# Optimization experiments

Measured on AMD Instinct MI355X. Metric: run time of the kernel, lower is better.

The kernel has to match this reference:

```python
import jax, jax.numpy as jnp
import numpy as np

B, T, N = 256, 512, 128  # batch, max seq len, num tags


def setup_inputs() -> dict:
    key = jax.random.key(0)
    k1, k2, k3, k4, k5, k6 = jax.random.split(key, 6)
    log_potentials = jax.random.normal(k1, (B, T, N), dtype=jnp.float32)
    transition = jax.random.normal(k2, (N, N), dtype=jnp.float32) * 0.01
    start_transition = jax.random.normal(k3, (N,), dtype=jnp.float32) * 0.01
    end_transition = jax.random.normal(k4, (N,), dtype=jnp.float32) * 0.01
    lengths = jax.random.randint(k5, (B,), T // 2, T + 1).astype(jnp.int32)
    target = jax.random.randint(k6, (B, T), 0, N).astype(jnp.int32)
    return {
        "log_potentials": log_potentials,
        "transition": transition,
        "start_transition": start_transition,
        "end_transition": end_transition,
        "target": target,
        "lengths": lengths,
    }


def _log_partitions(log_potentials, transition, start_transition, end_transition, lengths):
    # log-semiring forward algorithm over ragged (length-masked) sequences.
    emit = jnp.transpose(log_potentials, (1, 0, 2))  # [T, B, N]
    alpha0 = start_transition[None, :] + emit[0]     # log.mul(start, e_0)

    valid = (jnp.arange(1, emit.shape[0])[:, None] < lengths[None, :])  # [T-1, B]

    def step(alpha, inp):
        e_t, v_t = inp
        # log.vm: new[b, j] = logsumexp_i alpha[b, i] + transition[i, j] + e_t[b, j]
        new = jax.nn.logsumexp(alpha[:, :, None] + transition[None, :, :], axis=1) + e_t
        alpha = jnp.where(v_t[:, None], new, alpha)  # padded steps act as semiring unit
        return alpha, None

    alpha, _ = jax.lax.scan(step, alpha0, (emit[1:], valid))
    # log.mv with end transition
    return jax.nn.logsumexp(alpha + end_transition[None, :], axis=-1)  # [B]


def _log_scores(log_potentials, transition, start_transition, end_transition, target, lengths):
    Tn = log_potentials.shape[1]
    tidx = jnp.arange(Tn)
    valid = tidx[None, :] < lengths[:, None]  # [B, T]
    emis = jnp.take_along_axis(log_potentials, target[..., None].astype(jnp.int32), axis=-1)[..., 0]
    emis_score = jnp.sum(jnp.where(valid, emis, 0.0), axis=1)
    tr = transition[target[:, :-1], target[:, 1:]]
    tr_score = jnp.sum(jnp.where(valid[:, 1:], tr, 0.0), axis=1)
    last = jnp.take_along_axis(target, (lengths - 1)[:, None], axis=1)[:, 0]
    return emis_score + tr_score + start_transition[target[:, 0]] + end_transition[last]


def reference(log_potentials, transition, start_transition, end_transition, target, lengths):
    # CrfDecoderABC.fit -> CrfDistribution.log_prob = log_scores - log_partitions
    log_z = _log_partitions(log_potentials, transition, start_transition, end_transition, lengths)
    score = _log_scores(log_potentials, transition, start_transition, end_transition, target, lengths)
    return score - log_z  # [B]
```

## Files before the change

kernel.cpp:

```cpp
#include <hip/hip_runtime.h>

#define B_ 256
#define T_ 512
#define N_ 128

typedef float v2f __attribute__((ext_vector_type(2)));

__device__ __forceinline__ float readlane_f(float v, int k) {
    return __int_as_float(__builtin_amdgcn_readlane(__float_as_int(v), k));
}

__device__ __forceinline__ void barrier_lds() {
    asm volatile("s_waitcnt lgkmcnt(0)\n\ts_barrier" ::: "memory");
}

__global__ __launch_bounds__(256, 1) void crf_fused_kernel(
    const float* __restrict__ lp,
    const float* __restrict__ trans,
    const float* __restrict__ startt,
    const float* __restrict__ endt,
    const int*   __restrict__ target,
    const int*   __restrict__ lengths,
    float*       __restrict__ out)
{
    const int b   = blockIdx.x;
    const int tid = threadIdx.x;
    const int w   = tid >> 6;
    const int l   = tid & 63;
    const int lq  = l & 31;

    __shared__ v2f  part[2][4][64];
    __shared__ float red[8];

    const float* lpb = lp + (size_t)b * (T_ * N_);
    const int len = lengths[b];

    v2f e2[32];
    {
        const float* tq = trans + (w << 5) * N_;
        #pragma unroll
        for (int k = 0; k < 32; ++k) {
            e2[k] = (v2f){ __expf(tq[k * N_ + l]),
                           __expf(tq[k * N_ + 64 + l]) };
        }
    }

    float s = __expf(startt[(w << 5) + lq] + lpb[(w << 5) + lq]);

    float Macc = 0.f;

    const float* emb = lpb + (w << 5) + lq;
    float cur = emb[1 * N_], nA = emb[2 * N_], nB = emb[3 * N_];

    const int fi = ((((w & 1) << 5) + lq) << 1) + (w >> 1);

    for (int t = 1; t < len; ++t) {
        const int tp = min(t + 3, T_ - 1);
        float nn = emb[tp * N_];

        float eexp = __expf(cur);

        v2f a0 = {0.f, 0.f}, a1 = {0.f, 0.f}, a2 = {0.f, 0.f}, a3 = {0.f, 0.f};
        #pragma unroll
        for (int k = 0; k < 32; k += 4) {
            float x0 = readlane_f(s, k);
            float x1 = readlane_f(s, k + 1);
            float x2 = readlane_f(s, k + 2);
            float x3 = readlane_f(s, k + 3);
            a0 = __builtin_elementwise_fma(e2[k],     (v2f){x0, x0}, a0);
            a1 = __builtin_elementwise_fma(e2[k + 1], (v2f){x1, x1}, a1);
            a2 = __builtin_elementwise_fma(e2[k + 2], (v2f){x2, x2}, a2);
            a3 = __builtin_elementwise_fma(e2[k + 3], (v2f){x3, x3}, a3);
        }
        v2f p = (a0 + a1) + (a2 + a3);

        const int pb = t & 1;
        part[pb][w][l] = p;
        barrier_lds();

        const float* pbase = (const float*)&part[pb][0][0];
        float r0 = pbase[fi];
        float r1 = pbase[128 + fi];
        float r2 = pbase[256 + fi];
        float r3 = pbase[384 + fi];
        float sc4 = (r0 + r1) + (r2 + r3);

        if ((t & 3) == 0) {
            float scp = pbase[0];
            float isc = __builtin_amdgcn_rcpf(scp);
            sc4 *= isc;
            Macc += __logf(scp);
        }

        s = sc4 * eexp;

        cur = nA; nA = nB; nB = nn;
    }

    {
        float f = (l < 32) ? s * __expf(endt[(w << 5) + l]) : 0.f;
        #pragma unroll
        for (int off = 32; off > 0; off >>= 1) f += __shfl_xor(f, off);
        if (l == 0) red[w] = f;
    }

    const int* tg = target + b * T_;
    float acc = 0.f;
    for (int t = tid; t < len; t += 256) {
        int c = tg[t];
        acc += lpb[t * N_ + c];
        if (t + 1 < len) acc += trans[c * N_ + tg[t + 1]];
    }
    #pragma unroll
    for (int off = 32; off > 0; off >>= 1) acc += __shfl_xor(acc, off);
    if (l == 0) red[4 + w] = acc;
    __syncthreads();

    if (tid == 0) {
        float fz = (red[0] + red[1]) + (red[2] + red[3]);
        float sc = (red[4] + red[5]) + (red[6] + red[7]);
        out[b] = sc + startt[tg[0]] + endt[tg[len - 1]] - (Macc + __logf(fz));
    }
}

extern "C" void kernel_launch(void* const* d_in, const int* in_sizes, int n_in,
                              void* d_out, int out_size, void* d_ws, size_t ws_size,
                              hipStream_t stream) {
    const float* lp     = (const float*)d_in[0];
    const float* trans  = (const float*)d_in[1];
    const float* st     = (const float*)d_in[2];
    const float* en     = (const float*)d_in[3];
    const int*   target = (const int*)d_in[4];
    const int*   lens   = (const int*)d_in[5];
    float* out = (float*)d_out;

    crf_fused_kernel<<<B_, 256, 0, stream>>>(lp, trans, st, en, target, lens, out);
}
```

Baseline: 275.5 us.

## Run CRF forward recurrence on bf16 MFMA with expm1 transition split

Replaces the readlane-broadcast FP32 FMA matvec per time step with bf16 MFMA 16x16x32 instructions. The transition matrix is stored as expm1(trans) in bf16 and the identity part is added back exactly through the alpha sum (S*e), which keeps bf16 rounding error small. The state is exchanged through a small double-buffered LDS vector instead of partial-sum reduction, the loop is unrolled by two, and rescaling now uses an exponent-bit power-of-two shift in place of log/rcp. This cuts the VALU and readlane cost on the serial critical path, at the price of bf16 precision in the correction term and MFMA latency on each step.

```diff
diff --git a/kernel.cpp b/kernel.cpp
--- a/kernel.cpp
+++ b/kernel.cpp
@@ -4,12 +4,19 @@
 #define T_ 512
 #define N_ 128
 
-typedef float v2f __attribute__((ext_vector_type(2)));
+typedef float  f32x4 __attribute__((ext_vector_type(4)));
+typedef short  s16x8 __attribute__((ext_vector_type(8)));
+typedef unsigned int u32x4 __attribute__((ext_vector_type(4)));
 
-__device__ __forceinline__ float readlane_f(float v, int k) {
-    return __int_as_float(__builtin_amdgcn_readlane(__float_as_int(v), k));
+__device__ __forceinline__ unsigned int bf16_rne(float f) {
+    unsigned int u = __float_as_uint(f);
+    u += 0x7FFFu + ((u >> 16) & 1u);
+    return u >> 16;
 }
-
+__device__ __forceinline__ unsigned int pack_bf16(float lo, float hi) {
+    return __builtin_amdgcn_perm(__float_as_uint(hi), __float_as_uint(lo),
+                                 0x07060302u);
+}
 __device__ __forceinline__ void barrier_lds() {
     asm volatile("s_waitcnt lgkmcnt(0)\n\ts_barrier" ::: "memory");
 }
@@ -27,78 +34,101 @@
     const int tid = threadIdx.x;
     const int w   = tid >> 6;
     const int l   = tid & 63;
-    const int lq  = l & 31;
+    const int c   = l & 15;
+    const int g   = l >> 4;
+    const int gp  = g & 1;
 
-    __shared__ v2f  part[2][4][64];
+    __shared__ float xld[2][N_];
     __shared__ float red[8];
 
     const float* lpb = lp + (size_t)b * (T_ * N_);
     const int len = lengths[b];
 
-    v2f e2[32];
-    {
-        const float* tq = trans + (w << 5) * N_;
+    s16x8 Bf[4][2];
+    #pragma unroll
+    for (int kt = 0; kt < 4; ++kt) {
         #pragma unroll
-        for (int k = 0; k < 32; ++k) {
-            e2[k] = (v2f){ __expf(tq[k * N_ + l]),
-                           __expf(tq[k * N_ + 64 + l]) };
+        for (int jtl = 0; jtl < 2; ++jtl) {
+            const float* tq = trans + (32 * kt + 8 * g) * N_ + 16 * (2 * w + jtl) + c;
+            unsigned d0 = bf16_rne(expm1f(tq[0 * N_])) | (bf16_rne(expm1f(tq[1 * N_])) << 16);
+            unsigned d1 = bf16_rne(expm1f(tq[2 * N_])) | (bf16_rne(expm1f(tq[3 * N_])) << 16);
+            unsigned d2 = bf16_rne(expm1f(tq[4 * N_])) | (bf16_rne(expm1f(tq[5 * N_])) << 16);
+            unsigned d3 = bf16_rne(expm1f(tq[6 * N_])) | (bf16_rne(expm1f(tq[7 * N_])) << 16);
+            u32x4 u = { d0, d1, d2, d3 };
+            Bf[kt][jtl] = __builtin_bit_cast(s16x8, u);
         }
     }
 
-    float s = __expf(startt[(w << 5) + lq] + lpb[(w << 5) + lq]);
+    const int jsel = 32 * w + 16 * gp + c;
 
-    float Macc = 0.f;
+    float a_sel = __expf(startt[jsel] + lpb[jsel]);
+    if (l < 32) xld[0][32 * w + l] = a_sel;
 
-    const float* emb = lpb + (w << 5) + lq;
-    float cur = emb[1 * N_], nA = emb[2 * N_], nB = emb[3 * N_];
+    int Mexp = 0;
 
-    const int fi = ((((w & 1) << 5) + lq) << 1) + (w >> 1);
+    float emA = lpb[1 * N_ + jsel];
+    float emB = lpb[2 * N_ + jsel];
 
-    for (int t = 1; t < len; ++t) {
-        const int tp = min(t + 3, T_ - 1);
-        float nn = emb[tp * N_];
+    barrier_lds();
 
-        float eexp = __expf(cur);
+    auto step = [&](int t, float& em) {
+        const int pr = (t - 1) & 1;
+        const int pw = t & 1;
 
-        v2f a0 = {0.f, 0.f}, a1 = {0.f, 0.f}, a2 = {0.f, 0.f}, a3 = {0.f, 0.f};
+        s16x8 Af[4];
+        f32x4 sv = { 0.f, 0.f, 0.f, 0.f };
         #pragma unroll
-        for (int k = 0; k < 32; k += 4) {
-            float x0 = readlane_f(s, k);
-            float x1 = readlane_f(s, k + 1);
-            float x2 = readlane_f(s, k + 2);
-            float x3 = readlane_f(s, k + 3);
-            a0 = __builtin_elementwise_fma(e2[k],     (v2f){x0, x0}, a0);
-            a1 = __builtin_elementwise_fma(e2[k + 1], (v2f){x1, x1}, a1);
-            a2 = __builtin_elementwise_fma(e2[k + 2], (v2f){x2, x2}, a2);
-            a3 = __builtin_elementwise_fma(e2[k + 3], (v2f){x3, x3}, a3);
+        for (int kt = 0; kt < 4; ++kt) {
+            const f32x4* ls = (const f32x4*)&xld[pr][32 * kt + 8 * g];
+            f32x4 lo = ls[0], hi = ls[1];
+            sv += lo + hi;
+            u32x4 u = { pack_bf16(lo[0], lo[1]), pack_bf16(lo[2], lo[3]),
+                        pack_bf16(hi[0], hi[1]), pack_bf16(hi[2], hi[3]) };
+            Af[kt] = __builtin_bit_cast(s16x8, u);
         }
-        v2f p = (a0 + a1) + (a2 + a3);
+        float S = (sv[0] + sv[1]) + (sv[2] + sv[3]);
+        S += __shfl_xor(S, 16);
+        S += __shfl_xor(S, 32);
 
-        const int pb = t & 1;
-        part[pb][w][l] = p;
+        float ee = __expf(em);
+        em = lpb[(size_t)min(t + 2, T_ - 1) * N_ + jsel];
+
+        float e2 = ee;
+        if ((t & 3) == 0) {
+            unsigned eb = (__float_as_uint(S) >> 23) & 0xFFu;
+            e2 *= __uint_as_float((254u - eb) << 23);
+            Mexp += (int)eb - 127;
+        }
+        const float Se2 = S * e2;
+
+        f32x4 z = { 0.f, 0.f, 0.f, 0.f };
+        f32x4 p0 = __builtin_amdgcn_mfma_f32_16x16x32_bf16(Af[0], Bf[0][0], z, 0, 0, 0);
+        f32x4 p1 = __builtin_amdgcn_mfma_f32_16x16x32_bf16(Af[0], Bf[0][1], z, 0, 0, 0);
+        f32x4 q0 = __builtin_amdgcn_mfma_f32_16x16x32_bf16(Af[1], Bf[1][0], z, 0, 0, 0);
+        f32x4 q1 = __builtin_amdgcn_mfma_f32_16x16x32_bf16(Af[1], Bf[1][1], z, 0, 0, 0);
+        f32x4 r0 = __builtin_amdgcn_mfma_f32_16x16x32_bf16(Af[2], Bf[2][0], z, 0, 0, 0);
+        f32x4 r1 = __builtin_amdgcn_mfma_f32_16x16x32_bf16(Af[2], Bf[2][1], z, 0, 0, 0);
+        f32x4 s0 = __builtin_amdgcn_mfma_f32_16x16x32_bf16(Af[3], Bf[3][0], z, 0, 0, 0);
+        f32x4 s1 = __builtin_amdgcn_mfma_f32_16x16x32_bf16(Af[3], Bf[3][1], z, 0, 0, 0);
+        float y0 = (p0[0] + q0[0]) + (r0[0] + s0[0]);
+        float y1 = (p1[0] + q1[0]) + (r1[0] + s1[0]);
+
+        float ysel = gp ? y1 : y0;
+        a_sel = fmaf(ysel, e2, Se2);
+        if (l < 32) xld[pw][32 * w + l] = a_sel;
         barrier_lds();
+    };
 
-        const float* pbase = (const float*)&part[pb][0][0];
-        float r0 = pbase[fi];
-        float r1 = pbase[128 + fi];
-        float r2 = pbase[256 + fi];
-        float r3 = pbase[384 + fi];
-        float sc4 = (r0 + r1) + (r2 + r3);
-
-        if ((t & 3) == 0) {
-            float scp = pbase[0];
-            float isc = __builtin_amdgcn_rcpf(scp);
-            sc4 *= isc;
-            Macc += __logf(scp);
-        }
-
-        s = sc4 * eexp;
-
-        cur = nA; nA = nB; nB = nn;
+    int t = 1;
+    while (t + 1 < len) {
+        step(t, emA);
+        step(t + 1, emB);
+        t += 2;
     }
+    if (t < len) step(t, emA);
 
     {
-        float f = (l < 32) ? s * __expf(endt[(w << 5) + l]) : 0.f;
+        float f = (g < 2) ? a_sel * __expf(endt[jsel]) : 0.f;
         #pragma unroll
         for (int off = 32; off > 0; off >>= 1) f += __shfl_xor(f, off);
         if (l == 0) red[w] = f;
@@ -106,10 +136,10 @@
 
     const int* tg = target + b * T_;
     float acc = 0.f;
-    for (int t = tid; t < len; t += 256) {
-        int c = tg[t];
-        acc += lpb[t * N_ + c];
-        if (t + 1 < len) acc += trans[c * N_ + tg[t + 1]];
+    for (int t2 = tid; t2 < len; t2 += 256) {
+        int cc = tg[t2];
+        acc += lpb[t2 * N_ + cc];
+        if (t2 + 1 < len) acc += trans[cc * N_ + tg[t2 + 1]];
     }
     #pragma unroll
     for (int off = 32; off > 0; off >>= 1) acc += __shfl_xor(acc, off);
@@ -119,7 +149,8 @@
     if (tid == 0) {
         float fz = (red[0] + red[1]) + (red[2] + red[3]);
         float sc = (red[4] + red[5]) + (red[6] + red[7]);
-        out[b] = sc + startt[tg[0]] + endt[tg[len - 1]] - (Macc + __logf(fz));
+        out[b] = sc + startt[tg[0]] + endt[tg[len - 1]]
+               - ((float)Mexp * 0.69314718055994531f + __logf(fz));
     }
 }
 
```

Measured after the change: 290.5 us. 1.05x slower.
